# Kernel optimization log

Measured on AMD Instinct MI355X. Metric: run time of the kernel, lower is better.

## Reference

```python
import jax, jax.numpy as jnp
import numpy as np
import math

L, D, H, FF = 6, 512, 8, 2048
B, S = 8, 1024
EPS = 1e-5


def sin_pos_embedding(num_embeddings, dim, padding_idx=0):
    half = dim // 2
    freq = jnp.exp(jnp.arange(half, dtype=jnp.float32) * (-math.log(10000.0) / (half - 1)))
    ang = jnp.arange(num_embeddings, dtype=jnp.float32)[:, None] * freq[None, :]
    emb = jnp.concatenate([jnp.sin(ang), jnp.cos(ang)], axis=1)
    return emb.at[padding_idx].set(0.0)


def layer_norm(x, g, b):
    mu = jnp.mean(x, axis=-1, keepdims=True)
    var = jnp.mean(jnp.square(x - mu), axis=-1, keepdims=True)
    return (x - mu) * jax.lax.rsqrt(var + EPS) * g + b


def setup_inputs() -> dict:
    key = jax.random.key(0)
    ks = jax.random.split(key, 16)
    s = 0.02
    inp = {
        'x': jax.random.normal(ks[0], (B, S, D), jnp.float32),
        'char_ids': jax.random.randint(ks[1], (B, S), 0, 10000, jnp.int64) if jax.config.read('jax_enable_x64') else jax.random.randint(ks[1], (B, S), 0, 10000, jnp.int32),
        'seq_len': jnp.full((B,), S, jnp.int32),
        'mask': jnp.ones((B, S), jnp.int32),
        'Wqkv': jax.random.normal(ks[2], (L, D, 3 * D), jnp.float32) * s,
        'Wfc': jax.random.normal(ks[3], (L, D, D), jnp.float32) * s,
        'bfc': jnp.zeros((L, D), jnp.float32),
        'ln1_g': jnp.ones((L, D), jnp.float32), 'ln1_b': jnp.zeros((L, D), jnp.float32),
        'ln2_g': jnp.ones((L, D), jnp.float32), 'ln2_b': jnp.zeros((L, D), jnp.float32),
        'W1': jax.random.normal(ks[4], (L, D, FF), jnp.float32) * s,
        'b1': jnp.zeros((L, FF), jnp.float32),
        'W2': jax.random.normal(ks[5], (L, FF, D), jnp.float32) * s,
        'b2': jnp.zeros((L, D), jnp.float32),
    }
    return inp


def reference(x, char_ids, seq_len, mask, Wqkv, Wfc, bfc, ln1_g, ln1_b, ln2_g, ln2_b, W1, b1, W2, b2):
    # sinusoidal positional embedding computed from mask positions (padding_idx=0)
    valid = (mask != 0).astype(jnp.int32)
    positions = jnp.cumsum(valid, axis=1) * valid  # [B,S], pads -> 0
    table = sin_pos_embedding(S + 2, D)  # max_pos = padding_idx+1+S
    x = x + table[positions]

    key_mask = (mask == 0)[:, None, None, :]  # [B,1,1,S]
    dh = D // H

    for l in range(L):
        residual = x
        qkv = jnp.einsum('bsd,de->bse', x, Wqkv[l])  # [B,S,3D]
        q, k, v = jnp.split(qkv, 3, axis=-1)
        q = q.reshape(B, S, H, dh).transpose(0, 2, 1, 3)  # [B,H,S,dh]
        k = k.reshape(B, S, H, dh).transpose(0, 2, 1, 3)
        v = v.reshape(B, S, H, dh).transpose(0, 2, 1, 3)
        attn = jnp.einsum('bhqd,bhkd->bhqk', q, k)  # scale=1 (scale=False)
        attn = jnp.where(key_mask, -jnp.inf, attn)
        attn = jax.nn.softmax(attn, axis=-1)
        o = jnp.einsum('bhqk,bhkd->bhqd', attn, v)
        o = o.transpose(0, 2, 1, 3).reshape(B, S, D)
        o = jnp.einsum('bsd,de->bse', o, Wfc[l]) + bfc[l]
        x = layer_norm(o + residual, ln1_g[l], ln1_b[l])
        residual = x
        h = jax.nn.relu(jnp.einsum('bsd,df->bsf', x, W1[l]) + b1[l])
        h = jnp.einsum('bsf,fd->bsd', h, W2[l]) + b2[l]
        x = layer_norm(residual + h, ln2_g[l], ln2_b[l])
    return x
```

## Files before the change

kernel.cpp:

```cpp
#include <hip/hip_runtime.h>
#include <math.h>

#define LAYERS 6
#define DMODEL 512
#define NHEAD 8
#define DHEAD 64
#define FFDIM 2048
#define BATCH 8
#define SEQ 1024
#define ROWS (BATCH * SEQ)
#define EPS 1e-5f

typedef __attribute__((ext_vector_type(8))) short bf16x8;
typedef __attribute__((ext_vector_type(4))) float f32x4;

__device__ inline short f2bf(float f) {
    union { float f; unsigned u; } v; v.f = f;
    unsigned r = (v.u + 0x7FFFu + ((v.u >> 16) & 1u)) >> 16;
    return (short)r;
}

#define GLOAD_LDS16(g, l)                                                      \
    __builtin_amdgcn_global_load_lds(                                          \
        (__attribute__((address_space(1))) void*)(g),                          \
        (__attribute__((address_space(3))) void*)(l), 16, 0, 0)

__global__ void wtrans_kernel(const float* __restrict__ src, short* __restrict__ dst,
                              int K, int N) {
    __shared__ float t[32][33];
    const size_t mofs = (size_t)blockIdx.z * K * N;
    src += mofs; dst += mofs;
    int n0 = blockIdx.x * 32, k0 = blockIdx.y * 32;
    int tx = threadIdx.x, ty = threadIdx.y;
#pragma unroll
    for (int i = 0; i < 4; ++i)
        t[ty + 8 * i][tx] = src[(size_t)(k0 + ty + 8 * i) * N + n0 + tx];
    __syncthreads();
#pragma unroll
    for (int i = 0; i < 4; ++i)
        dst[(size_t)(n0 + ty + 8 * i) * K + k0 + tx] = f2bf(t[tx][ty + 8 * i]);
}

__global__ void pos_scan_kernel(const int* __restrict__ mask, int* __restrict__ pos) {
    __shared__ int sm[SEQ];
    int b = blockIdx.x;
    int t = threadIdx.x;
    int v = (mask[b * SEQ + t] != 0) ? 1 : 0;
    sm[t] = v;
    __syncthreads();
    for (int off = 1; off < SEQ; off <<= 1) {
        int add = (t >= off) ? sm[t - off] : 0;
        __syncthreads();
        sm[t] += add;
        __syncthreads();
    }
    pos[b * SEQ + t] = sm[t] * v;
}

__global__ void add_pos_kernel(const float* __restrict__ xin, const int* __restrict__ pos,
                               float* __restrict__ xout, short* __restrict__ xb) {
    int bs = blockIdx.x;
    int t = threadIdx.x;
    int p = pos[bs];
    int d0 = t * 4;
    const float C = -logf(10000.0f) * (1.0f / 255.0f);
    float4 xv = *(const float4*)(xin + (size_t)bs * DMODEL + d0);
    float e[4];
#pragma unroll
    for (int j = 0; j < 4; ++j) {
        int d = d0 + j;
        if (p == 0) {
            e[j] = 0.0f;
        } else {
            int dd = (d < 256) ? d : d - 256;
            float freq = expf((float)dd * C);
            float ang = (float)p * freq;
            e[j] = (d < 256) ? sinf(ang) : cosf(ang);
        }
    }
    float4 ov;
    ov.x = xv.x + e[0]; ov.y = xv.y + e[1]; ov.z = xv.z + e[2]; ov.w = xv.w + e[3];
    *(float4*)(xout + (size_t)bs * DMODEL + d0) = ov;
    short4 sb;
    sb.x = f2bf(ov.x); sb.y = f2bf(ov.y); sb.z = f2bf(ov.z); sb.w = f2bf(ov.w);
    *(short4*)(xb + (size_t)bs * DMODEL + d0) = sb;
}


template <bool OUTBF16, bool BIAS, bool RELU>
__global__ __launch_bounds__(256) void gemm_bf16_kernel(const short* __restrict__ A,
                                                        const short* __restrict__ BT,
                                                        const float* __restrict__ bias,
                                                        void* __restrict__ Cv,
                                                        int M, int N, int K) {
    __shared__ __attribute__((aligned(16))) short Asm[2][128 * 32];
    __shared__ __attribute__((aligned(16))) short Bsm[2][128 * 32];
    const int tid = threadIdx.x;
    const int w = tid >> 6;
    const int lane = tid & 63;
    const int quad = lane >> 4;
    const int lr = lane & 15;
    const int m0 = blockIdx.y * 128;
    const int n0 = blockIdx.x * 128;
    const int wm = (w >> 1) * 64;
    const int wn = (w & 1) * 64;

    const int segr = lane >> 2;
    const int segk = (((lane & 3) - (lane >> 3)) & 3) * 8;
    const int sA0 = w * 2, sA1 = w * 2 + 1;
    const short* gA0 = A + (size_t)(m0 + sA0 * 16 + segr) * K + segk;
    const short* gA1 = A + (size_t)(m0 + sA1 * 16 + segr) * K + segk;
    const short* gB0 = BT + (size_t)(n0 + sA0 * 16 + segr) * K + segk;
    const short* gB1 = BT + (size_t)(n0 + sA1 * 16 + segr) * K + segk;
    const int lofs0 = sA0 * 512 + lane * 8;
    const int lofs1 = sA1 * 512 + lane * 8;
    const int gp = ((quad + (lr >> 1)) & 3) * 8;

    f32x4 acc[4][4];
#pragma unroll
    for (int i = 0; i < 4; ++i)
#pragma unroll
        for (int j = 0; j < 4; ++j) { acc[i][j][0] = 0.f; acc[i][j][1] = 0.f; acc[i][j][2] = 0.f; acc[i][j][3] = 0.f; }

    GLOAD_LDS16(gA0, &Asm[0][lofs0]);
    GLOAD_LDS16(gA1, &Asm[0][lofs1]);
    GLOAD_LDS16(gB0, &Bsm[0][lofs0]);
    GLOAD_LDS16(gB1, &Bsm[0][lofs1]);

    const int nk = K >> 5;
    for (int i = 0; i < nk; ++i) {
        __syncthreads();
        if (i + 1 < nk) {
            const int k1 = (i + 1) * 32;
            const int nb = (i + 1) & 1;
            GLOAD_LDS16(gA0 + k1, &Asm[nb][lofs0]);
            GLOAD_LDS16(gA1 + k1, &Asm[nb][lofs1]);
            GLOAD_LDS16(gB0 + k1, &Bsm[nb][lofs0]);
            GLOAD_LDS16(gB1 + k1, &Bsm[nb][lofs1]);
        }
        const int cur = i & 1;
        bf16x8 af[4], bfr[4];
#pragma unroll
        for (int mt = 0; mt < 4; ++mt)
            af[mt] = *(const bf16x8*)&Asm[cur][(wm + mt * 16 + lr) * 32 + gp];
#pragma unroll
        for (int nt = 0; nt < 4; ++nt)
            bfr[nt] = *(const bf16x8*)&Bsm[cur][(wn + nt * 16 + lr) * 32 + gp];
#pragma unroll
        for (int mt = 0; mt < 4; ++mt)
#pragma unroll
            for (int nt = 0; nt < 4; ++nt)
                acc[mt][nt] = __builtin_amdgcn_mfma_f32_16x16x32_bf16(af[mt], bfr[nt], acc[mt][nt], 0, 0, 0);
    }

    float bv[4];
    if (BIAS) {
#pragma unroll
        for (int nt = 0; nt < 4; ++nt) bv[nt] = bias[n0 + wn + nt * 16 + lr];
    }
#pragma unroll
    for (int mt = 0; mt < 4; ++mt)
#pragma unroll
        for (int nt = 0; nt < 4; ++nt)
#pragma unroll
            for (int r = 0; r < 4; ++r) {
                float v = acc[mt][nt][r];
                if (BIAS) v += bv[nt];
                if (RELU) v = fmaxf(v, 0.f);
                int row = m0 + wm + mt * 16 + quad * 4 + r;
                int col = n0 + wn + nt * 16 + lr;
                if (OUTBF16)
                    ((short*)Cv)[(size_t)row * N + col] = f2bf(v);
                else
                    ((float*)Cv)[(size_t)row * N + col] = v;
            }
}

template <bool OUTBF16, bool BIAS, bool RELU>
__global__ __launch_bounds__(256) void gemm_bf16_m64_kernel(const short* __restrict__ A,
                                                            const short* __restrict__ BT,
                                                            const float* __restrict__ bias,
                                                            void* __restrict__ Cv,
                                                            int M, int N, int K) {
    __shared__ __attribute__((aligned(16))) short Asm[2][64 * 32];
    __shared__ __attribute__((aligned(16))) short Bsm[2][128 * 32];
    const int tid = threadIdx.x;
    const int w = tid >> 6;
    const int lane = tid & 63;
    const int quad = lane >> 4;
    const int lr = lane & 15;
    const int m0 = blockIdx.y * 64;
    const int n0 = blockIdx.x * 128;
    const int wm = (w >> 1) * 32;
    const int wn = (w & 1) * 64;

    const int segr = lane >> 2;
    const int segk = (((lane & 3) - (lane >> 3)) & 3) * 8;
    const short* gA  = A + (size_t)(m0 + w * 16 + segr) * K + segk;
    const short* gB0 = BT + (size_t)(n0 + (2 * w) * 16 + segr) * K + segk;
    const short* gB1 = BT + (size_t)(n0 + (2 * w + 1) * 16 + segr) * K + segk;
    const int lA  = w * 512 + lane * 8;
    const int lB0 = (2 * w) * 512 + lane * 8;
    const int lB1 = (2 * w + 1) * 512 + lane * 8;
    const int gp = ((quad + (lr >> 1)) & 3) * 8;

    f32x4 acc[2][4];
#pragma unroll
    for (int i = 0; i < 2; ++i)
#pragma unroll
        for (int j = 0; j < 4; ++j) { acc[i][j][0] = 0.f; acc[i][j][1] = 0.f; acc[i][j][2] = 0.f; acc[i][j][3] = 0.f; }

    GLOAD_LDS16(gA, &Asm[0][lA]);
    GLOAD_LDS16(gB0, &Bsm[0][lB0]);
    GLOAD_LDS16(gB1, &Bsm[0][lB1]);

    const int nk = K >> 5;
    for (int i = 0; i < nk; ++i) {
        __syncthreads();
        if (i + 1 < nk) {
            const int k1 = (i + 1) * 32;
            const int nb = (i + 1) & 1;
            GLOAD_LDS16(gA + k1, &Asm[nb][lA]);
            GLOAD_LDS16(gB0 + k1, &Bsm[nb][lB0]);
            GLOAD_LDS16(gB1 + k1, &Bsm[nb][lB1]);
        }
        const int cur = i & 1;
        bf16x8 af[2], bfr[4];
#pragma unroll
        for (int mt = 0; mt < 2; ++mt)
            af[mt] = *(const bf16x8*)&Asm[cur][(wm + mt * 16 + lr) * 32 + gp];
#pragma unroll
        for (int nt = 0; nt < 4; ++nt)
            bfr[nt] = *(const bf16x8*)&Bsm[cur][(wn + nt * 16 + lr) * 32 + gp];
#pragma unroll
        for (int mt = 0; mt < 2; ++mt)
#pragma unroll
            for (int nt = 0; nt < 4; ++nt)
                acc[mt][nt] = __builtin_amdgcn_mfma_f32_16x16x32_bf16(af[mt], bfr[nt], acc[mt][nt], 0, 0, 0);
    }

    float bv[4];
    if (BIAS) {
#pragma unroll
        for (int nt = 0; nt < 4; ++nt) bv[nt] = bias[n0 + wn + nt * 16 + lr];
    }
#pragma unroll
    for (int mt = 0; mt < 2; ++mt)
#pragma unroll
        for (int nt = 0; nt < 4; ++nt)
#pragma unroll
            for (int r = 0; r < 4; ++r) {
                float v = acc[mt][nt][r];
                if (BIAS) v += bv[nt];
                if (RELU) v = fmaxf(v, 0.f);
                int row = m0 + wm + mt * 16 + quad * 4 + r;
                int col = n0 + wn + nt * 16 + lr;
                if (OUTBF16)
                    ((short*)Cv)[(size_t)row * N + col] = f2bf(v);
                else
                    ((float*)Cv)[(size_t)row * N + col] = v;
            }
}

#define QTILE 256
__global__ __launch_bounds__(512) void attn_mfma_kernel(const short* __restrict__ qkv,
                                                        const int* __restrict__ mask,
                                                        short* __restrict__ o) {
    __shared__ __attribute__((aligned(16))) short Ks[2][64][72];
    __shared__ __attribute__((aligned(16))) short Vt[2][64][72];
    __shared__ __attribute__((aligned(16))) short Ps[8][16][72];
    __shared__ float Msf[2][64];

    const int qt = blockIdx.x;
    const int bh = blockIdx.y;
    const int b = bh >> 3, h = bh & 7;
    const int tid = threadIdx.x;
    const int w = tid >> 6;
    const int lane = tid & 63;
    const int quad = lane >> 4;
    const int lr = lane & 15;
    const size_t seqrow = (size_t)b * SEQ;

    bf16x8 qf[2][2];
#pragma unroll
    for (int mt = 0; mt < 2; ++mt)
#pragma unroll
        for (int c = 0; c < 2; ++c)
            qf[mt][c] = *(const bf16x8*)(qkv +
                (seqrow + qt * QTILE + w * 32 + mt * 16 + lr) * (3 * DMODEL)
                + h * DHEAD + c * 32 + quad * 8);

    const bool isK = (tid < 256);
    const int st = isK ? tid : tid - 256;
    const int kkey = st >> 2;
    const int kg = (st & 3) * 8;
    const int vkp = st & 31;
    const int vdg = st >> 5;
    const short* gK = qkv + (seqrow + kkey) * (3 * DMODEL) + DMODEL + h * DHEAD + kg;
    const short* gV = qkv + (seqrow + 2 * vkp) * (3 * DMODEL) + 2 * DMODEL + h * DHEAD + vdg * 8;

    bf16x8 r0, r1;
    int mreg = 0;

    {
        if (isK) {
            r0 = *(const bf16x8*)(gK);
            r1 = *(const bf16x8*)(gK + 32);
        } else {
            r0 = *(const bf16x8*)(gV);
            r1 = *(const bf16x8*)(gV + 3 * DMODEL);
        }
        if (tid < 64) mreg = mask[seqrow + tid];
        if (isK) {
            *(bf16x8*)&Ks[0][kkey][kg] = r0;
            *(bf16x8*)&Ks[0][kkey][kg + 32] = r1;
        } else {
#pragma unroll
            for (int i = 0; i < 8; ++i) {
                short2 p; p.x = r0[i]; p.y = r1[i];
                *(short2*)&Vt[0][vdg * 8 + i][vkp * 2] = p;
            }
        }
        if (tid < 64) Msf[0][tid] = mreg ? 1.0f : 0.0f;
    }
    __syncthreads();

    f32x4 Oacc[2][4];
    float rs[2][4];
#pragma unroll
    for (int mt = 0; mt < 2; ++mt)
#pragma unroll
        for (int t2 = 0; t2 < 4; ++t2) { Oacc[mt][t2][0] = 0.f; Oacc[mt][t2][1] = 0.f; Oacc[mt][t2][2] = 0.f; Oacc[mt][t2][3] = 0.f; }
#pragma unroll
    for (int mt = 0; mt < 2; ++mt)
#pragma unroll
        for (int r = 0; r < 4; ++r) rs[mt][r] = 0.f;

    for (int kt = 0; kt < 16; ++kt) {
        const int cur = kt & 1;
        {
            const size_t ofs = (size_t)((kt + 1) & 15) * 64 * (3 * DMODEL);
            if (isK) {
                r0 = *(const bf16x8*)(gK + ofs);
                r1 = *(const bf16x8*)(gK + ofs + 32);
            } else {
                r0 = *(const bf16x8*)(gV + ofs);
                r1 = *(const bf16x8*)(gV + ofs + 3 * DMODEL);
            }
            if (tid < 64) mreg = mask[seqrow + ((kt + 1) & 15) * 64 + tid];
        }
        bf16x8 kf[2][4], vf[2][4];
#pragma unroll
        for (int c = 0; c < 2; ++c)
#pragma unroll
            for (int t = 0; t < 4; ++t) {
                kf[c][t] = *(const bf16x8*)&Ks[cur][lr + 16 * t][quad * 8 + 32 * c];
                vf[c][t] = *(const bf16x8*)&Vt[cur][lr + 16 * t][quad * 8 + 32 * c];
            }
        float mv[4];
#pragma unroll
        for (int t = 0; t < 4; ++t) mv[t] = Msf[cur][lr + 16 * t];

#pragma unroll
        for (int mt = 0; mt < 2; ++mt) {
            f32x4 S[4];
#pragma unroll
            for (int t = 0; t < 4; ++t) { S[t][0] = 0.f; S[t][1] = 0.f; S[t][2] = 0.f; S[t][3] = 0.f; }
#pragma unroll
            for (int c = 0; c < 2; ++c)
#pragma unroll
                for (int t = 0; t < 4; ++t)
                    S[t] = __builtin_amdgcn_mfma_f32_16x16x32_bf16(qf[mt][c], kf[c][t], S[t], 0, 0, 0);
#pragma unroll
            for (int t = 0; t < 4; ++t)
#pragma unroll
                for (int r = 0; r < 4; ++r) {
                    float p = __expf(S[t][r] - 8.0f) * mv[t];
                    S[t][r] = p;
                    rs[mt][r] += p;
                }
#pragma unroll
            for (int t = 0; t < 4; ++t)
#pragma unroll
                for (int r = 0; r < 4; ++r)
                    Ps[w][quad * 4 + r][lr + 16 * t] = f2bf(S[t][r]);
            bf16x8 pa0 = *(const bf16x8*)&Ps[w][lr][quad * 8];
            bf16x8 pa1 = *(const bf16x8*)&Ps[w][lr][quad * 8 + 32];
#pragma unroll
            for (int t2 = 0; t2 < 4; ++t2) {
                Oacc[mt][t2] = __builtin_amdgcn_mfma_f32_16x16x32_bf16(pa0, vf[0][t2], Oacc[mt][t2], 0, 0, 0);
                Oacc[mt][t2] = __builtin_amdgcn_mfma_f32_16x16x32_bf16(pa1, vf[1][t2], Oacc[mt][t2], 0, 0, 0);
            }
        }
        {
            const int nb = cur ^ 1;
            if (isK) {
                *(bf16x8*)&Ks[nb][kkey][kg] = r0;
                *(bf16x8*)&Ks[nb][kkey][kg + 32] = r1;
            } else {
#pragma unroll
                for (int i = 0; i < 8; ++i) {
                    short2 p; p.x = r0[i]; p.y = r1[i];
                    *(short2*)&Vt[nb][vdg * 8 + i][vkp * 2] = p;
                }
            }
            if (tid < 64) Msf[nb][tid] = mreg ? 1.0f : 0.0f;
        }
        __syncthreads();
    }

#pragma unroll
    for (int mt = 0; mt < 2; ++mt) {
        float inv[4];
#pragma unroll
        for (int r = 0; r < 4; ++r) {
            float v = rs[mt][r];
            v += __shfl_xor(v, 1);
            v += __shfl_xor(v, 2);
            v += __shfl_xor(v, 4);
            v += __shfl_xor(v, 8);
            inv[r] = 1.f / v;
        }
#pragma unroll
        for (int t2 = 0; t2 < 4; ++t2)
#pragma unroll
            for (int r = 0; r < 4; ++r) {
                int row = qt * QTILE + w * 32 + mt * 16 + quad * 4 + r;
                o[(seqrow + row) * DMODEL + h * DHEAD + 16 * t2 + lr] = f2bf(Oacc[mt][t2][r] * inv[r]);
            }
    }
}

__global__ __launch_bounds__(64) void ln_kernel(const float* __restrict__ tmp,
                                                float* __restrict__ x,
                                                short* __restrict__ xb,
                                                const float* __restrict__ g,
                                                const float* __restrict__ bta) {
    const int row = blockIdx.x;
    const int t = threadIdx.x;
    const size_t base = (size_t)row * DMODEL + t * 8;
    float4 x0 = *(const float4*)(x + base);
    float4 x1 = *(const float4*)(x + base + 4);
    float4 t0 = *(const float4*)(tmp + base);
    float4 t1 = *(const float4*)(tmp + base + 4);
    float v[8];
    v[0] = x0.x + t0.x; v[1] = x0.y + t0.y; v[2] = x0.z + t0.z; v[3] = x0.w + t0.w;
    v[4] = x1.x + t1.x; v[5] = x1.y + t1.y; v[6] = x1.z + t1.z; v[7] = x1.w + t1.w;
    float s = 0.f, sq = 0.f;
#pragma unroll
    for (int i = 0; i < 8; ++i) { s += v[i]; sq += v[i] * v[i]; }
#pragma unroll
    for (int off = 1; off < 64; off <<= 1) {
        s += __shfl_xor(s, off);
        sq += __shfl_xor(sq, off);
    }
    float mu = s * (1.0f / DMODEL);
    float var = sq * (1.0f / DMODEL) - mu * mu;
    float r = rsqrtf(var + EPS);
    float4 g0 = *(const float4*)(g + t * 8);
    float4 g1 = *(const float4*)(g + t * 8 + 4);
    float4 b0 = *(const float4*)(bta + t * 8);
    float4 b1 = *(const float4*)(bta + t * 8 + 4);
    float ov[8];
    ov[0] = (v[0] - mu) * r * g0.x + b0.x;
    ov[1] = (v[1] - mu) * r * g0.y + b0.y;
    ov[2] = (v[2] - mu) * r * g0.z + b0.z;
    ov[3] = (v[3] - mu) * r * g0.w + b0.w;
    ov[4] = (v[4] - mu) * r * g1.x + b1.x;
    ov[5] = (v[5] - mu) * r * g1.y + b1.y;
    ov[6] = (v[6] - mu) * r * g1.z + b1.z;
    ov[7] = (v[7] - mu) * r * g1.w + b1.w;
    *(float4*)(x + base) = *(float4*)&ov[0];
    *(float4*)(x + base + 4) = *(float4*)&ov[4];
    bf16x8 ob;
#pragma unroll
    for (int i = 0; i < 8; ++i) ob[i] = f2bf(ov[i]);
    *(bf16x8*)(xb + base) = ob;
}

extern "C" void kernel_launch(void* const* d_in, const int* in_sizes, int n_in,
                              void* d_out, int out_size, void* d_ws, size_t ws_size,
                              hipStream_t stream) {
    const float* x_in  = (const float*)d_in[0];
    const int*   mask  = (const int*)d_in[3];
    const float* Wqkv  = (const float*)d_in[4];
    const float* Wfc   = (const float*)d_in[5];
    const float* bfc   = (const float*)d_in[6];
    const float* ln1_g = (const float*)d_in[7];
    const float* ln1_b = (const float*)d_in[8];
    const float* ln2_g = (const float*)d_in[9];
    const float* ln2_b = (const float*)d_in[10];
    const float* W1    = (const float*)d_in[11];
    const float* b1    = (const float*)d_in[12];
    const float* W2    = (const float*)d_in[13];
    const float* b2    = (const float*)d_in[14];

    float* x = (float*)d_out;

    char* ws = (char*)d_ws;
    size_t ofs = 0;
    int*   pos   = (int*)ws;                 ofs += 65536;
    float* tmp   = (float*)(ws + ofs);       ofs += (size_t)ROWS * DMODEL * 4;
    short* xb    = (short*)(ws + ofs);       ofs += (size_t)ROWS * DMODEL * 2;
    short* qkvb  = (short*)(ws + ofs);
    short* hb    = (short*)(ws + ofs);
    ofs += (size_t)ROWS * 3 * DMODEL * 2;
    short* obuf  = (short*)(ws + ofs);       ofs += (size_t)ROWS * DMODEL * 2;
    short* WqkvT = (short*)(ws + ofs);       ofs += (size_t)LAYERS * DMODEL * 3 * DMODEL * 2;
    short* WfcT  = (short*)(ws + ofs);       ofs += (size_t)LAYERS * DMODEL * DMODEL * 2;
    short* W1T   = (short*)(ws + ofs);       ofs += (size_t)LAYERS * DMODEL * FFDIM * 2;
    short* W2T   = (short*)(ws + ofs);       ofs += (size_t)LAYERS * FFDIM * DMODEL * 2;

    wtrans_kernel<<<dim3(3 * DMODEL / 32, DMODEL / 32, LAYERS), dim3(32, 8), 0, stream>>>(
        Wqkv, WqkvT, DMODEL, 3 * DMODEL);
    wtrans_kernel<<<dim3(DMODEL / 32, DMODEL / 32, LAYERS), dim3(32, 8), 0, stream>>>(
        Wfc, WfcT, DMODEL, DMODEL);
    wtrans_kernel<<<dim3(FFDIM / 32, DMODEL / 32, LAYERS), dim3(32, 8), 0, stream>>>(
        W1, W1T, DMODEL, FFDIM);
    wtrans_kernel<<<dim3(DMODEL / 32, FFDIM / 32, LAYERS), dim3(32, 8), 0, stream>>>(
        W2, W2T, FFDIM, DMODEL);

    pos_scan_kernel<<<BATCH, SEQ, 0, stream>>>(mask, pos);
    add_pos_kernel<<<ROWS, 128, 0, stream>>>(x_in, pos, x, xb);

    for (int l = 0; l < LAYERS; ++l) {
        const short* wqkvT_l = WqkvT + (size_t)l * DMODEL * 3 * DMODEL;
        const short* wfcT_l  = WfcT + (size_t)l * DMODEL * DMODEL;
        const short* w1T_l   = W1T + (size_t)l * DMODEL * FFDIM;
        const short* w2T_l   = W2T + (size_t)l * FFDIM * DMODEL;
        const float* bfc_l   = bfc + (size_t)l * DMODEL;
        const float* b1_l    = b1 + (size_t)l * FFDIM;
        const float* b2_l    = b2 + (size_t)l * DMODEL;

        gemm_bf16_kernel<true, false, false><<<dim3(3 * DMODEL / 128, ROWS / 128), 256, 0, stream>>>(
            xb, wqkvT_l, nullptr, qkvb, ROWS, 3 * DMODEL, DMODEL);
        attn_mfma_kernel<<<dim3(SEQ / QTILE, BATCH * NHEAD), 512, 0, stream>>>(qkvb, mask, obuf);
        gemm_bf16_m64_kernel<false, true, false><<<dim3(DMODEL / 128, ROWS / 64), 256, 0, stream>>>(
            obuf, wfcT_l, bfc_l, tmp, ROWS, DMODEL, DMODEL);
        ln_kernel<<<ROWS, 64, 0, stream>>>(tmp, x, xb, ln1_g + (size_t)l * DMODEL,
                                           ln1_b + (size_t)l * DMODEL);
        gemm_bf16_kernel<true, true, true><<<dim3(FFDIM / 128, ROWS / 128), 256, 0, stream>>>(
            xb, w1T_l, b1_l, hb, ROWS, FFDIM, DMODEL);
        gemm_bf16_m64_kernel<false, true, false><<<dim3(DMODEL / 128, ROWS / 64), 256, 0, stream>>>(
            hb, w2T_l, b2_l, tmp, ROWS, DMODEL, FFDIM);
        ln_kernel<<<ROWS, 64, 0, stream>>>(tmp, x, xb, ln2_g + (size_t)l * DMODEL,
                                           ln2_b + (size_t)l * DMODEL);
    }
}
```

Baseline: 1.108 ms.

## Halve attention query tile and compute transposed scores for packed P stores

The attention kernel now uses a 128-row query tile, so each wave handles 16 query rows instead of 32, with a launch-bounds hint of 4 blocks per CU. Scores are computed as K·Q^T, so each lane owns one query row. That lets the mask load as a vector, pack probabilities with v_cvt_pk_bf16_f32 into 8-byte LDS stores, and shrink the final row-sum reduction. The aim is lower register pressure, higher occupancy and cheaper softmax/P staging. The cost is that K/V tiles are reloaded twice as often per query, since each tile is reused by fewer query rows.

```diff
diff --git a/kernel.cpp b/kernel.cpp
--- a/kernel.cpp
+++ b/kernel.cpp
@@ -262,10 +262,10 @@
             }
 }
 
-#define QTILE 256
-__global__ __launch_bounds__(512) void attn_mfma_kernel(const short* __restrict__ qkv,
-                                                        const int* __restrict__ mask,
-                                                        short* __restrict__ o) {
+#define QTILE 128
+__global__ __launch_bounds__(512, 4) void attn_mfma_kernel(const short* __restrict__ qkv,
+                                                           const int* __restrict__ mask,
+                                                           short* __restrict__ o) {
     __shared__ __attribute__((aligned(16))) short Ks[2][64][72];
     __shared__ __attribute__((aligned(16))) short Vt[2][64][72];
     __shared__ __attribute__((aligned(16))) short Ps[8][16][72];
@@ -281,14 +281,12 @@
     const int lr = lane & 15;
     const size_t seqrow = (size_t)b * SEQ;
 
-    bf16x8 qf[2][2];
-#pragma unroll
-    for (int mt = 0; mt < 2; ++mt)
-#pragma unroll
-        for (int c = 0; c < 2; ++c)
-            qf[mt][c] = *(const bf16x8*)(qkv +
-                (seqrow + qt * QTILE + w * 32 + mt * 16 + lr) * (3 * DMODEL)
-                + h * DHEAD + c * 32 + quad * 8);
+    bf16x8 qf[2];
+#pragma unroll
+    for (int c = 0; c < 2; ++c)
+        qf[c] = *(const bf16x8*)(qkv +
+            (seqrow + qt * QTILE + w * 16 + lr) * (3 * DMODEL)
+            + h * DHEAD + c * 32 + quad * 8);
 
     const bool isK = (tid < 256);
     const int st = isK ? tid : tid - 256;
@@ -325,16 +323,10 @@
     }
     __syncthreads();
 
-    f32x4 Oacc[2][4];
-    float rs[2][4];
-#pragma unroll
-    for (int mt = 0; mt < 2; ++mt)
-#pragma unroll
-        for (int t2 = 0; t2 < 4; ++t2) { Oacc[mt][t2][0] = 0.f; Oacc[mt][t2][1] = 0.f; Oacc[mt][t2][2] = 0.f; Oacc[mt][t2][3] = 0.f; }
-#pragma unroll
-    for (int mt = 0; mt < 2; ++mt)
-#pragma unroll
-        for (int r = 0; r < 4; ++r) rs[mt][r] = 0.f;
+    f32x4 Oacc[4];
+    float rs = 0.f;
+#pragma unroll
+    for (int t2 = 0; t2 < 4; ++t2) { Oacc[t2][0] = 0.f; Oacc[t2][1] = 0.f; Oacc[t2][2] = 0.f; Oacc[t2][3] = 0.f; }
 
     for (int kt = 0; kt < 16; ++kt) {
         const int cur = kt & 1;
@@ -357,41 +349,38 @@
                 kf[c][t] = *(const bf16x8*)&Ks[cur][lr + 16 * t][quad * 8 + 32 * c];
                 vf[c][t] = *(const bf16x8*)&Vt[cur][lr + 16 * t][quad * 8 + 32 * c];
             }
-        float mv[4];
-#pragma unroll
-        for (int t = 0; t < 4; ++t) mv[t] = Msf[cur][lr + 16 * t];
-
-#pragma unroll
-        for (int mt = 0; mt < 2; ++mt) {
-            f32x4 S[4];
-#pragma unroll
-            for (int t = 0; t < 4; ++t) { S[t][0] = 0.f; S[t][1] = 0.f; S[t][2] = 0.f; S[t][3] = 0.f; }
-#pragma unroll
-            for (int c = 0; c < 2; ++c)
-#pragma unroll
-                for (int t = 0; t < 4; ++t)
-                    S[t] = __builtin_amdgcn_mfma_f32_16x16x32_bf16(qf[mt][c], kf[c][t], S[t], 0, 0, 0);
+
+        f32x4 S[4];
+#pragma unroll
+        for (int t = 0; t < 4; ++t) { S[t][0] = 0.f; S[t][1] = 0.f; S[t][2] = 0.f; S[t][3] = 0.f; }
+#pragma unroll
+        for (int c = 0; c < 2; ++c)
 #pragma unroll
             for (int t = 0; t < 4; ++t)
-#pragma unroll
-                for (int r = 0; r < 4; ++r) {
-                    float p = __expf(S[t][r] - 8.0f) * mv[t];
-                    S[t][r] = p;
-                    rs[mt][r] += p;
-                }
-#pragma unroll
-            for (int t = 0; t < 4; ++t)
-#pragma unroll
-                for (int r = 0; r < 4; ++r)
-                    Ps[w][quad * 4 + r][lr + 16 * t] = f2bf(S[t][r]);
-            bf16x8 pa0 = *(const bf16x8*)&Ps[w][lr][quad * 8];
-            bf16x8 pa1 = *(const bf16x8*)&Ps[w][lr][quad * 8 + 32];
-#pragma unroll
-            for (int t2 = 0; t2 < 4; ++t2) {
-                Oacc[mt][t2] = __builtin_amdgcn_mfma_f32_16x16x32_bf16(pa0, vf[0][t2], Oacc[mt][t2], 0, 0, 0);
-                Oacc[mt][t2] = __builtin_amdgcn_mfma_f32_16x16x32_bf16(pa1, vf[1][t2], Oacc[mt][t2], 0, 0, 0);
-            }
-        }
+                S[t] = __builtin_amdgcn_mfma_f32_16x16x32_bf16(kf[c][t], qf[c], S[t], 0, 0, 0);
+
+#pragma unroll
+        for (int t = 0; t < 4; ++t) {
+            f32x4 mvv = *(const f32x4*)&Msf[cur][16 * t + 4 * quad];
+            float p0 = __expf(S[t][0] - 8.0f) * mvv[0];
+            float p1 = __expf(S[t][1] - 8.0f) * mvv[1];
+            float p2 = __expf(S[t][2] - 8.0f) * mvv[2];
+            float p3 = __expf(S[t][3] - 8.0f) * mvv[3];
+            rs += (p0 + p1) + (p2 + p3);
+            unsigned lo, hi;
+            asm("v_cvt_pk_bf16_f32 %0, %1, %2" : "=v"(lo) : "v"(p0), "v"(p1));
+            asm("v_cvt_pk_bf16_f32 %0, %1, %2" : "=v"(hi) : "v"(p2), "v"(p3));
+            uint2 pk; pk.x = lo; pk.y = hi;
+            *(uint2*)&Ps[w][lr][16 * t + 4 * quad] = pk;
+        }
+        bf16x8 pa0 = *(const bf16x8*)&Ps[w][lr][quad * 8];
+        bf16x8 pa1 = *(const bf16x8*)&Ps[w][lr][quad * 8 + 32];
+#pragma unroll
+        for (int t2 = 0; t2 < 4; ++t2) {
+            Oacc[t2] = __builtin_amdgcn_mfma_f32_16x16x32_bf16(pa0, vf[0][t2], Oacc[t2], 0, 0, 0);
+            Oacc[t2] = __builtin_amdgcn_mfma_f32_16x16x32_bf16(pa1, vf[1][t2], Oacc[t2], 0, 0, 0);
+        }
+
         {
             const int nb = cur ^ 1;
             if (isK) {
@@ -409,26 +398,20 @@
         __syncthreads();
     }
 
-#pragma unroll
-    for (int mt = 0; mt < 2; ++mt) {
-        float inv[4];
+    rs += __shfl_xor(rs, 16);
+    rs += __shfl_xor(rs, 32);
+    float inv[4];
+#pragma unroll
+    for (int r = 0; r < 4; ++r)
+        inv[r] = 1.f / __shfl(rs, quad * 4 + r);
+
+#pragma unroll
+    for (int t2 = 0; t2 < 4; ++t2)
 #pragma unroll
         for (int r = 0; r < 4; ++r) {
-            float v = rs[mt][r];
-            v += __shfl_xor(v, 1);
-            v += __shfl_xor(v, 2);
-            v += __shfl_xor(v, 4);
-            v += __shfl_xor(v, 8);
-            inv[r] = 1.f / v;
-        }
-#pragma unroll
-        for (int t2 = 0; t2 < 4; ++t2)
-#pragma unroll
-            for (int r = 0; r < 4; ++r) {
-                int row = qt * QTILE + w * 32 + mt * 16 + quad * 4 + r;
-                o[(seqrow + row) * DMODEL + h * DHEAD + 16 * t2 + lr] = f2bf(Oacc[mt][t2][r] * inv[r]);
-            }
-    }
+            int row = qt * QTILE + w * 16 + quad * 4 + r;
+            o[(seqrow + row) * DMODEL + h * DHEAD + 16 * t2 + lr] = f2bf(Oacc[t2][r] * inv[r]);
+        }
 }
 
 __global__ __launch_bounds__(64) void ln_kernel(const float* __restrict__ tmp,
```

Measured after the change: 1.096 ms. About the same (-1.1%).
